# Optimization experiments

Hardware: AMD Instinct MI355X
Metric: run time of the kernel (lower is better)

## Reference

```python
import jax, jax.numpy as jnp
import numpy as np

B, V, N, S, F, H, K, STEPS = 8, 3, 400, 1200, 16, 32, 10, 12
ALPHA_FUSE = 0.8
NEG = -9e15


def setup_inputs() -> dict:
    key = jax.random.key(0)
    ks = jax.random.split(key, 16)
    g = lambda i, shape, s=0.1: jax.random.normal(ks[i], shape, jnp.float32) * s
    return {
        "feat": jax.random.normal(ks[0], (B, S, F), jnp.float32),
        "adj": jax.random.bernoulli(ks[1], 0.05, (B, V, S, S)).astype(jnp.float32),
        "dis_lab": jax.random.uniform(ks[2], (B, K), dtype=jnp.float32),
        "W_gat": g(3, (V, F, H), 0.3),
        "a_gat": g(4, (V, 2 * H, 1), 0.3),
        "qkv_W": g(5, (H, 3 * H)),
        "qkv_b": jnp.zeros((3 * H,), jnp.float32),
        "o_W": g(6, (H, H)),
        "o_b": jnp.zeros((H,), jnp.float32),
        "fus_W": g(7, (H, H)),
        "fus_b": jnp.zeros((H,), jnp.float32),
        "att1_W": g(8, (2 * H, H)),
        "att1_b": jnp.zeros((H,), jnp.float32),
        "att2_W": g(9, (H, 1)),
        "att2_b": jnp.zeros((1,), jnp.float32),
        "gru_Wih": g(10, (H, 3 * H)),
        "gru_Whh": g(11, (H, 3 * H)),
        "gru_bih": jnp.zeros((3 * H,), jnp.float32),
        "gru_bhh": jnp.zeros((3 * H,), jnp.float32),
        "out_W": g(12, (H, 1)),
        "out_b": jnp.zeros((1,), jnp.float32),
    }


def _forward(feat, adj, dis_lab, W_gat, a_gat, qkv_W, qkv_b, o_W, o_b,
             fus_W, fus_b, att1_W, att1_b, att2_W, att2_b,
             gru_Wih, gru_Whh, gru_bih, gru_bhh, out_W, out_b):
    # ---- per-view GAT (masked softmax over dense adjacency) ----
    Wh = jnp.einsum('bsf,vfh->bvsh', feat, W_gat)            # [B,V,S,H]
    a1, a2 = a_gat[:, :H, 0], a_gat[:, H:, 0]
    e = (jnp.einsum('bvsh,vh->bvs', Wh, a1)[..., :, None]
         + jnp.einsum('bvsh,vh->bvs', Wh, a2)[..., None, :])  # [B,V,S,S]
    e = jax.nn.leaky_relu(e, 0.2)
    e = jnp.where(adj > 0, e, NEG)
    att = jax.nn.softmax(e, axis=-1)
    hid = jax.nn.elu(jnp.einsum('bvst,bvth->bvsh', att, Wh))  # [B,V,S,H]
    # ---- cross-view self-attention fusion (single head) ----
    x = hid.reshape(B, V * S, H)
    q, k, v = jnp.split(x @ qkv_W + qkv_b, 3, axis=-1)
    logits = jnp.einsum('bld,bmd->blm', q, k) / jnp.sqrt(jnp.float32(H))
    sa = jnp.einsum('blm,bmd->bld', jax.nn.softmax(logits, axis=-1), v)
    sa = sa @ o_W + o_b
    hfuse = (ALPHA_FUSE * sa + (1.0 - ALPHA_FUSE) * x).reshape(B, V, S, H)
    gate = jax.nn.sigmoid(hfuse @ fus_W + fus_b)
    fusion = jnp.sum(gate * hfuse, axis=1)[:, 2 * N:, :]      # [B,N,H]
    # ---- attention over label stations ----
    label = fusion[:, :K, :]                                  # [B,K,H]
    unlabel = fusion[:, K, :]                                 # [B,H]
    cat = jnp.concatenate([label, jnp.broadcast_to(unlabel[:, None, :], label.shape)], axis=-1)
    s = jax.nn.relu(cat @ att1_W + att1_b) @ att2_W + att2_b  # [B,K,1]
    score = jax.nn.softmax(s[..., 0] * dis_lab, axis=1)
    ctx = jnp.einsum('bk,bkh->bh', score, label)
    # ---- GRU decoder (feed hidden state back as next input) ----
    def gru_cell(xt, h):
        gi = xt @ gru_Wih + gru_bih
        gh = h @ gru_Whh + gru_bhh
        ir, iz, inn = jnp.split(gi, 3, axis=-1)
        hr, hz, hn = jnp.split(gh, 3, axis=-1)
        r = jax.nn.sigmoid(ir + hr)
        z = jax.nn.sigmoid(iz + hz)
        n = jnp.tanh(inn + r * hn)
        return (1.0 - z) * n + z * h
    def step(carry, _):
        xt, h = carry
        h2 = gru_cell(xt, h)
        out = h2 @ out_W + out_b
        return (h2, h2), out[:, 0]
    _, outs = jax.lax.scan(step, (ctx, unlabel), None, length=STEPS)
    return outs.T  # [B, STEPS]


def reference(feat, adj, dis_lab, W_gat, a_gat, qkv_W, qkv_b, o_W, o_b,
              fus_W, fus_b, att1_W, att1_b, att2_W, att2_b,
              gru_Wih, gru_Whh, gru_bih, gru_bhh, out_W, out_b):
    return _forward(feat, adj, dis_lab, W_gat, a_gat, qkv_W, qkv_b, o_W, o_b,
                    fus_W, fus_b, att1_W, att1_b, att2_W, att2_b,
                    gru_Wih, gru_Whh, gru_bih, gru_bhh, out_W, out_b)
```

## Files before the change

kernel.cpp:

```cpp
#include <hip/hip_runtime.h>
#include <math.h>

#define Bb 8
#define Vv 3
#define Ss 1200
#define Ff 16
#define Hh 32
#define Kk 10
#define STEPS 12
#define ROWS (Bb*Vv*Ss)
#define L (Vv*Ss)
#define KPAD 1216

typedef __attribute__((ext_vector_type(8))) short bf16x8;
typedef __attribute__((ext_vector_type(4))) float f32x4;
typedef __attribute__((ext_vector_type(4))) unsigned int u32x4;

__device__ __forceinline__ unsigned int pack_hi2(float x0, float x1) {
    return (__float_as_uint(x1) & 0xFFFF0000u) | (__float_as_uint(x0) >> 16);
}
__device__ __forceinline__ unsigned int pack_lo2(float x0, float x1) {
    float h0 = __uint_as_float(__float_as_uint(x0) & 0xFFFF0000u);
    float h1 = __uint_as_float(__float_as_uint(x1) & 0xFFFF0000u);
    return (__float_as_uint(x1 - h1) & 0xFFFF0000u) | (__float_as_uint(x0 - h0) >> 16);
}

__global__ __launch_bounds__(256) void gat_wh_k(const float* __restrict__ feat,
                                                const float* __restrict__ W_gat,
                                                const float* __restrict__ a_gat,
                                                float* __restrict__ Wh,
                                                float* __restrict__ fvec,
                                                float* __restrict__ gvec) {
    int blk = blockIdx.x;
    int c = blk % 150;
    int v = (blk / 150) % Vv;
    int b = blk / (150 * Vv);
    int tid = threadIdx.x;
    int r = tid >> 5;
    int h = tid & 31;
    int s = c * 8 + r;

    __shared__ float Wg[16][32];
    __shared__ float fe[8][16];
    for (int i = tid; i < 512; i += 256) Wg[i >> 5][i & 31] = W_gat[v * 512 + i];
    for (int i = tid; i < 128; i += 256) fe[i >> 4][i & 15] = feat[(b * Ss + c * 8) * Ff + i];
    __syncthreads();

    float acc = 0.f;
#pragma unroll
    for (int k = 0; k < 16; ++k) acc += fe[r][k] * Wg[k][h];

    int row = (b * Vv + v) * Ss + s;
    Wh[(size_t)row * Hh + h] = acc;

    float a1 = a_gat[v * 64 + h];
    float a2 = a_gat[v * 64 + 32 + h];
    float pf = acc * a1, pg = acc * a2;
#pragma unroll
    for (int m = 16; m >= 1; m >>= 1) {
        pf += __shfl_xor(pf, m);
        pg += __shfl_xor(pg, m);
    }
    if (h == 0) { fvec[row] = pf; gvec[row] = pg; }
}

__global__ __launch_bounds__(256) void gmax_k(const float* __restrict__ gvec,
                                              float* __restrict__ Gmax) {
    int bv = blockIdx.x;
    int tid = threadIdx.x;
    float m = -3.0e38f;
    for (int t = tid; t < Ss; t += 256) m = fmaxf(m, gvec[bv * Ss + t]);
#pragma unroll
    for (int mm = 32; mm >= 1; mm >>= 1) m = fmaxf(m, __shfl_xor(m, mm));
    __shared__ float red[4];
    if ((tid & 63) == 0) red[tid >> 6] = m;
    __syncthreads();
    if (tid == 0) Gmax[bv] = fmaxf(fmaxf(red[0], red[1]), fmaxf(red[2], red[3]));
}

__global__ __launch_bounds__(256) void wht_k(const float* __restrict__ Wh,
                                             ushort* __restrict__ WhT_hi,
                                             ushort* __restrict__ WhT_lo) {
    int bv = blockIdx.x / 19, t = blockIdx.x % 19;
    int s0 = t * 64;
    int tid = threadIdx.x;
    __shared__ float T[64][33];
    for (int idx = tid; idx < 2048; idx += 256) {
        int r = idx >> 5, h = idx & 31;
        T[r][h] = (s0 + r < Ss) ? Wh[((size_t)bv * Ss + s0 + r) * Hh + h] : 0.f;
    }
    __syncthreads();
    int h = tid >> 3, c = tid & 7;
    unsigned int hb[4], lb[4];
#pragma unroll
    for (int j = 0; j < 4; ++j) {
        float e0 = T[c * 8 + 2 * j][h], e1 = T[c * 8 + 2 * j + 1][h];
        hb[j] = pack_hi2(e0, e1);
        lb[j] = pack_lo2(e0, e1);
    }
    size_t off = ((size_t)bv * 32 + h) * KPAD + s0 + c * 8;
    *(uint4*)(WhT_hi + off) = make_uint4(hb[0], hb[1], hb[2], hb[3]);
    *(uint4*)(WhT_lo + off) = make_uint4(lb[0], lb[1], lb[2], lb[3]);
}

__global__ __launch_bounds__(128) void wsplit_k(const float* __restrict__ qkv_W,
                                                ushort* __restrict__ WqT_hi,
                                                ushort* __restrict__ WqT_lo) {
    int n = threadIdx.x;
    if (n < 96) {
        for (int k = 0; k < 32; ++k) {
            float w = qkv_W[k * 96 + n];
            unsigned int u = __float_as_uint(w);
            float hf = __uint_as_float(u & 0xFFFF0000u);
            WqT_hi[n * 32 + k] = (ushort)(u >> 16);
            WqT_lo[n * 32 + k] = (ushort)(__float_as_uint(w - hf) >> 16);
        }
    }
}

__global__ __launch_bounds__(128) void gat_mfma_k(const float* __restrict__ adj,
                                                  const ushort* __restrict__ WhT_hi,
                                                  const ushort* __restrict__ WhT_lo,
                                                  const float* __restrict__ fvec,
                                                  const float* __restrict__ gvec,
                                                  const float* __restrict__ Gmax,
                                                  const ushort* __restrict__ WqT_hi,
                                                  const ushort* __restrict__ WqT_lo,
                                                  const float* __restrict__ qkv_b,
                                                  float* __restrict__ KV,
                                                  float* __restrict__ qsel,
                                                  float* __restrict__ hsel) {
    int blk = blockIdx.x;
    int bv = blk / 38, tb = blk % 38;
    int wave = threadIdx.x >> 6, lane = threadIdx.x & 63;
    int rowbase = tb * 32 + wave * 16;
    int lr = lane & 15, kg = lane >> 4;
    int b = bv / Vv, v = bv - b * Vv;

    int ar = rowbase + lr;
    int ar_c = (ar < Ss) ? ar : (Ss - 1);
    const float* adj_r = adj + ((size_t)bv * Ss + ar_c) * Ss;
    const float* g_b = gvec + (size_t)bv * Ss;
    float fr = fvec[bv * Ss + ar_c];
    float M = fr + Gmax[bv];
    float Mr = fmaxf(M, 0.2f * M);

    f32x4 acc0 = {0.f, 0.f, 0.f, 0.f}, acc1 = {0.f, 0.f, 0.f, 0.f};
    float psum = 0.f;
    const ushort* Bh0 = WhT_hi + ((size_t)bv * 32 + lr) * KPAD;
    const ushort* Bl0 = WhT_lo + ((size_t)bv * 32 + lr) * KPAD;

    for (int k0 = 0; k0 < KPAD; k0 += 32) {
        int t0 = k0 + kg * 8;
        bf16x8 bh0 = *(const bf16x8*)(Bh0 + t0);
        bf16x8 bl0 = *(const bf16x8*)(Bl0 + t0);
        bf16x8 bh1 = *(const bf16x8*)(Bh0 + 16 * KPAD + t0);
        bf16x8 bl1 = *(const bf16x8*)(Bl0 + 16 * KPAD + t0);

        float p[8];
        if (t0 < Ss) {
            float4 aA = *(const float4*)(adj_r + t0);
            float4 aB = *(const float4*)(adj_r + t0 + 4);
            float4 gA = *(const float4*)(g_b + t0);
            float4 gB = *(const float4*)(g_b + t0 + 4);
            float av[8] = {aA.x, aA.y, aA.z, aA.w, aB.x, aB.y, aB.z, aB.w};
            float gv[8] = {gA.x, gA.y, gA.z, gA.w, gB.x, gB.y, gB.z, gB.w};
#pragma unroll
            for (int j = 0; j < 8; ++j) {
                float e = fr + gv[j];
                e = fmaxf(e, 0.2f * e);
                float pe = __expf(e - Mr);
                p[j] = (av[j] > 0.f) ? pe : 0.f;
                psum += p[j];
            }
        } else {
#pragma unroll
            for (int j = 0; j < 8; ++j) p[j] = 0.f;
        }
        unsigned int hb[4], lb[4];
#pragma unroll
        for (int j = 0; j < 4; ++j) {
            hb[j] = pack_hi2(p[2 * j], p[2 * j + 1]);
            lb[j] = pack_lo2(p[2 * j], p[2 * j + 1]);
        }
        bf16x8 ah = __builtin_bit_cast(bf16x8, (u32x4){hb[0], hb[1], hb[2], hb[3]});
        bf16x8 al = __builtin_bit_cast(bf16x8, (u32x4){lb[0], lb[1], lb[2], lb[3]});
        acc0 = __builtin_amdgcn_mfma_f32_16x16x32_bf16(ah, bh0, acc0, 0, 0, 0);
        acc0 = __builtin_amdgcn_mfma_f32_16x16x32_bf16(ah, bl0, acc0, 0, 0, 0);
        acc0 = __builtin_amdgcn_mfma_f32_16x16x32_bf16(al, bh0, acc0, 0, 0, 0);
        acc1 = __builtin_amdgcn_mfma_f32_16x16x32_bf16(ah, bh1, acc1, 0, 0, 0);
        acc1 = __builtin_amdgcn_mfma_f32_16x16x32_bf16(ah, bl1, acc1, 0, 0, 0);
        acc1 = __builtin_amdgcn_mfma_f32_16x16x32_bf16(al, bh1, acc1, 0, 0, 0);
    }

    psum += __shfl_xor(psum, 16);
    psum += __shfl_xor(psum, 32);

    __shared__ float hidS[2][16][36];
#pragma unroll
    for (int j = 0; j < 4; ++j) {
        float ps = __shfl(psum, kg * 4 + j);
        float r0 = acc0[j] / ps;
        float r1 = acc1[j] / ps;
        hidS[wave][kg * 4 + j][lr]      = (r0 > 0.f) ? r0 : expm1f(r0);
        hidS[wave][kg * 4 + j][16 + lr] = (r1 > 0.f) ? r1 : expm1f(r1);
    }
    __syncthreads();

    float4 h4a = *(const float4*)&hidS[wave][lr][8 * kg];
    float4 h4b = *(const float4*)&hidS[wave][lr][8 * kg + 4];
    float hv[8] = {h4a.x, h4a.y, h4a.z, h4a.w, h4b.x, h4b.y, h4b.z, h4b.w};
    unsigned int hhb[4], hlb[4];
#pragma unroll
    for (int j = 0; j < 4; ++j) {
        hhb[j] = pack_hi2(hv[2 * j], hv[2 * j + 1]);
        hlb[j] = pack_lo2(hv[2 * j], hv[2 * j + 1]);
    }
    bf16x8 ahh = __builtin_bit_cast(bf16x8, (u32x4){hhb[0], hhb[1], hhb[2], hhb[3]});
    bf16x8 ahl = __builtin_bit_cast(bf16x8, (u32x4){hlb[0], hlb[1], hlb[2], hlb[3]});

#pragma unroll
    for (int t = 0; t < 4; ++t) {
        int n = 32 + t * 16 + lr;
        bf16x8 wh = *(const bf16x8*)(WqT_hi + n * 32 + 8 * kg);
        bf16x8 wl = *(const bf16x8*)(WqT_lo + n * 32 + 8 * kg);
        float bias = qkv_b[n];
        f32x4 qa = {bias, bias, bias, bias};
        qa = __builtin_amdgcn_mfma_f32_16x16x32_bf16(ahh, wh, qa, 0, 0, 0);
        qa = __builtin_amdgcn_mfma_f32_16x16x32_bf16(ahh, wl, qa, 0, 0, 0);
        qa = __builtin_amdgcn_mfma_f32_16x16x32_bf16(ahl, wh, qa, 0, 0, 0);
#pragma unroll
        for (int j = 0; j < 4; ++j) {
            int row = rowbase + kg * 4 + j;
            if (row < Ss)
                KV[((size_t)b * L + v * Ss + row) * 64 + t * 16 + lr] = qa[j];
        }
    }
    if (rowbase == 800) {
#pragma unroll
        for (int t = 0; t < 2; ++t) {
            int n = t * 16 + lr;
            bf16x8 wh = *(const bf16x8*)(WqT_hi + n * 32 + 8 * kg);
            bf16x8 wl = *(const bf16x8*)(WqT_lo + n * 32 + 8 * kg);
            float bias = qkv_b[n];
            f32x4 qa = {bias, bias, bias, bias};
            qa = __builtin_amdgcn_mfma_f32_16x16x32_bf16(ahh, wh, qa, 0, 0, 0);
            qa = __builtin_amdgcn_mfma_f32_16x16x32_bf16(ahh, wl, qa, 0, 0, 0);
            qa = __builtin_amdgcn_mfma_f32_16x16x32_bf16(ahl, wh, qa, 0, 0, 0);
#pragma unroll
            for (int j = 0; j < 4; ++j) {
                int si = kg * 4 + j;
                if (si < 11)
                    qsel[((size_t)b * 33 + si * 3 + v) * 32 + t * 16 + lr] = qa[j];
            }
        }
#pragma unroll
        for (int j = 0; j < 4; ++j) {
            int si = kg * 4 + j;
            if (si < 11) {
                hsel[(((size_t)b * Vv + v) * 11 + si) * 32 + lr]      = hidS[wave][si][lr];
                hsel[(((size_t)b * Vv + v) * 11 + si) * 32 + 16 + lr] = hidS[wave][si][16 + lr];
            }
        }
    }
}

#define CH 120
#define NCH 30
#define PREC 34
__global__ __launch_bounds__(256) void attn_part_k(const float* __restrict__ KV,
                                                   const float* __restrict__ qsel,
                                                   float* __restrict__ part) {
    int blk = blockIdx.x;
    int b = blk / NCH, ch = blk % NCH;
    int k0 = ch * CH;
    int tid = threadIdx.x;
    const float inv = 0.1767766952966369f;

    __shared__ float qS[33][33];
    __shared__ float kS[CH][33];
    __shared__ float lS[33][124];
    __shared__ float mS[33], lsS[33];

    for (int idx = tid; idx < 33 * 32; idx += 256) {
        int q = idx >> 5, i = idx & 31;
        qS[q][i] = qsel[((size_t)b * 33 + q) * 32 + i];
    }
    for (int idx = tid; idx < CH * 32; idx += 256) {
        int r = idx >> 5, i = idx & 31;
        kS[r][i] = KV[((size_t)b * L + k0 + r) * 64 + i];
    }
    __syncthreads();

    for (int idx = tid; idx < 33 * CH; idx += 256) {
        int q = idx / CH, k = idx - q * CH;
        float d = 0.f;
#pragma unroll
        for (int i = 0; i < 32; ++i) d += qS[q][i] * kS[k][i];
        lS[q][k] = d * inv;
    }
    __syncthreads();

    int q4 = tid >> 2, j4 = tid & 3;
    if (q4 < 33) {
        float m = -3.0e38f;
        for (int k = j4; k < CH; k += 4) m = fmaxf(m, lS[q4][k]);
        m = fmaxf(m, __shfl_xor(m, 1));
        m = fmaxf(m, __shfl_xor(m, 2));
        float ssum = 0.f;
        for (int k = j4; k < CH; k += 4) {
            float p = __expf(lS[q4][k] - m);
            lS[q4][k] = p;
            ssum += p;
        }
        ssum += __shfl_xor(ssum, 1);
        ssum += __shfl_xor(ssum, 2);
        if (j4 == 0) { mS[q4] = m; lsS[q4] = ssum; }
    }
    __syncthreads();

    for (int idx = tid; idx < CH * 32; idx += 256) {
        int r = idx >> 5, i = idx & 31;
        kS[r][i] = KV[((size_t)b * L + k0 + r) * 64 + 32 + i];
    }
    __syncthreads();

    float* po = part + ((size_t)b * NCH + ch) * (33 * PREC);
    for (int idx = tid; idx < 33 * 32; idx += 256) {
        int q = idx >> 5, hh = idx & 31;
        float a = 0.f;
        for (int k = 0; k < CH; k += 4) {
            float4 p4 = *(const float4*)&lS[q][k];
            a += p4.x * kS[k][hh] + p4.y * kS[k+1][hh] + p4.z * kS[k+2][hh] + p4.w * kS[k+3][hh];
        }
        po[q * PREC + hh] = a;
    }
    if (tid < 33) { po[tid * PREC + 32] = mS[tid]; po[tid * PREC + 33] = lsS[tid]; }
}

__global__ __launch_bounds__(256) void attn_comb_k(const float* __restrict__ part,
                                                   const float* __restrict__ hsel,
                                                   const float* __restrict__ o_W,
                                                   const float* __restrict__ o_b,
                                                   const float* __restrict__ fus_W,
                                                   const float* __restrict__ fus_b,
                                                   float* __restrict__ hfg) {
    int b = blockIdx.x;
    int tid = threadIdx.x;
    __shared__ float RS[33][NCH];
    __shared__ float LSs[33];
    __shared__ float oS[33][33];
    __shared__ float hfS[33][33];
    const float* pb = part + (size_t)b * NCH * (33 * PREC);

    if (tid < 33) {
        float M = -3.0e38f;
        for (int c = 0; c < NCH; ++c) M = fmaxf(M, pb[c * 33 * PREC + tid * PREC + 32]);
        float Lt = 0.f;
        for (int c = 0; c < NCH; ++c) {
            float w = __expf(pb[c * 33 * PREC + tid * PREC + 32] - M);
            RS[tid][c] = w;
            Lt += w * pb[c * 33 * PREC + tid * PREC + 33];
        }
        LSs[tid] = Lt;
    }
    __syncthreads();

    for (int idx = tid; idx < 33 * 32; idx += 256) {
        int q = idx >> 5, hh = idx & 31;
        float a = 0.f;
        for (int c = 0; c < NCH; ++c) a += RS[q][c] * pb[c * 33 * PREC + q * PREC + hh];
        oS[q][hh] = a / LSs[q];
    }
    __syncthreads();
    for (int idx = tid; idx < 33 * 32; idx += 256) {
        int q = idx >> 5, hh = idx & 31;
        int si = q / 3, v = q - si * 3;
        float o = o_b[hh];
#pragma unroll
        for (int i = 0; i < 32; ++i) o += oS[q][i] * o_W[i * 32 + hh];
        float x = hsel[(((size_t)b * Vv + v) * 11 + si) * Hh + hh];
        hfS[q][hh] = 0.8f * o + 0.2f * x;
    }
    __syncthreads();
    for (int idx = tid; idx < 33 * 32; idx += 256) {
        int q = idx >> 5, hh = idx & 31;
        float gacc = fus_b[hh];
#pragma unroll
        for (int i = 0; i < 32; ++i) gacc += hfS[q][i] * fus_W[i * 32 + hh];
        float gate = 1.f / (1.f + __expf(-gacc));
        hfg[(size_t)(b * 33 + q) * 32 + hh] = gate * hfS[q][hh];
    }
}

__global__ __launch_bounds__(64) void head_k(const float* __restrict__ hfg,
                                             const float* __restrict__ dis_lab,
                                             const float* __restrict__ att1_W,
                                             const float* __restrict__ att1_b,
                                             const float* __restrict__ att2_W,
                                             const float* __restrict__ att2_b,
                                             const float* __restrict__ Wih,
                                             const float* __restrict__ Whh,
                                             const float* __restrict__ bih,
                                             const float* __restrict__ bhh,
                                             const float* __restrict__ out_W,
                                             const float* __restrict__ out_b,
                                             float* __restrict__ out) {
    int b = blockIdx.x;
    int tid = threadIdx.x;
    int j = tid & 31, half = tid >> 5;

    __shared__ float lab[11][32];
    __shared__ float a1T[32][68];
    __shared__ float WihT[3][32][36];
    __shared__ float WhhT[3][32][36];
    __shared__ float sc[12];
    __shared__ float xS[32], hS[32];

    for (int i = tid; i < 352; i += 64) {
        int k = i >> 5, hh = i & 31;
        float val = 0.f;
#pragma unroll
        for (int v = 0; v < 3; ++v) val += hfg[(size_t)(b * 33 + k * 3 + v) * 32 + hh];
        lab[k][hh] = val;
    }
    for (int idx = tid; idx < 2048; idx += 64) {
        int i = idx >> 5, jj = idx & 31;
        a1T[jj][i] = att1_W[idx];
    }
    for (int idx = tid; idx < 3072; idx += 64) {
        int i = idx / 96, col = idx - i * 96;
        int g = col >> 5, jj = col & 31;
        WihT[g][jj][i] = Wih[idx];
        WhhT[g][jj][i] = Whh[idx];
    }
    __syncthreads();

    float a2w = att2_W[j];
    float a1b = att1_b[j];
    float a2b = att2_b[0];
#pragma unroll
    for (int kk = 0; kk < 5; ++kk) {
        int k = 2 * kk + half;
        float t1 = a1b;
#pragma unroll
        for (int c = 0; c < 8; ++c) {
            float4 lb4 = *(const float4*)&lab[k][c * 4];
            float4 w4  = *(const float4*)&a1T[j][c * 4];
            t1 += lb4.x * w4.x + lb4.y * w4.y + lb4.z * w4.z + lb4.w * w4.w;
        }
#pragma unroll
        for (int c = 0; c < 8; ++c) {
            float4 lb4 = *(const float4*)&lab[10][c * 4];
            float4 w4  = *(const float4*)&a1T[j][32 + c * 4];
            t1 += lb4.x * w4.x + lb4.y * w4.y + lb4.z * w4.z + lb4.w * w4.w;
        }
        float val = fmaxf(t1, 0.f) * a2w;
#pragma unroll
        for (int mm = 16; mm >= 1; mm >>= 1) val += __shfl_xor(val, mm);
        if (j == 0) sc[k] = (val + a2b) * dis_lab[b * Kk + k];
    }
    __syncthreads();
    if (tid == 0) {
        float mx = sc[0];
        for (int k = 1; k < 10; ++k) mx = fmaxf(mx, sc[k]);
        float sm = 0.f;
        for (int k = 0; k < 10; ++k) { sc[k] = __expf(sc[k] - mx); sm += sc[k]; }
        for (int k = 0; k < 10; ++k) sc[k] /= sm;
    }
    __syncthreads();
    if (tid < 32) {
        float c = 0.f;
        for (int k = 0; k < 10; ++k) c += sc[k] * lab[k][tid];
        xS[tid] = c;
        hS[tid] = lab[10][tid];
    }
    __syncthreads();

    float b_ir = bih[j], b_iz = bih[32 + j], b_in = bih[64 + j];
    float b_hr = bhh[j], b_hz = bhh[32 + j], b_hn = bhh[64 + j];
    float ow = out_W[j], ob = out_b[0];
    int i0 = half * 16;

    for (int t = 0; t < STEPS; ++t) {
        float gi_r = 0.f, gi_z = 0.f, gi_n = 0.f;
        float gh_r = 0.f, gh_z = 0.f, gh_n = 0.f;
#pragma unroll
        for (int c = 0; c < 4; ++c) {
            float4 x4 = *(const float4*)&xS[i0 + c * 4];
            float4 h4 = *(const float4*)&hS[i0 + c * 4];
            float4 wr = *(const float4*)&WihT[0][j][i0 + c * 4];
            float4 wz = *(const float4*)&WihT[1][j][i0 + c * 4];
            float4 wn = *(const float4*)&WihT[2][j][i0 + c * 4];
            float4 ur = *(const float4*)&WhhT[0][j][i0 + c * 4];
            float4 uz = *(const float4*)&WhhT[1][j][i0 + c * 4];
            float4 un = *(const float4*)&WhhT[2][j][i0 + c * 4];
            gi_r += x4.x * wr.x + x4.y * wr.y + x4.z * wr.z + x4.w * wr.w;
            gi_z += x4.x * wz.x + x4.y * wz.y + x4.z * wz.z + x4.w * wz.w;
            gi_n += x4.x * wn.x + x4.y * wn.y + x4.z * wn.z + x4.w * wn.w;
            gh_r += h4.x * ur.x + h4.y * ur.y + h4.z * ur.z + h4.w * ur.w;
            gh_z += h4.x * uz.x + h4.y * uz.y + h4.z * uz.z + h4.w * uz.w;
            gh_n += h4.x * un.x + h4.y * un.y + h4.z * un.z + h4.w * un.w;
        }
        gi_r += __shfl_xor(gi_r, 32); gi_z += __shfl_xor(gi_z, 32); gi_n += __shfl_xor(gi_n, 32);
        gh_r += __shfl_xor(gh_r, 32); gh_z += __shfl_xor(gh_z, 32); gh_n += __shfl_xor(gh_n, 32);

        float hprev = hS[j];
        float r = 1.f / (1.f + __expf(-(gi_r + b_ir + gh_r + b_hr)));
        float z = 1.f / (1.f + __expf(-(gi_z + b_iz + gh_z + b_hz)));
        float n = tanhf(gi_n + b_in + r * (gh_n + b_hn));
        float hnew = (1.f - z) * n + z * hprev;

        float outp = hnew * ow;
#pragma unroll
        for (int mm = 16; mm >= 1; mm >>= 1) outp += __shfl_xor(outp, mm);
        if (tid == 0) out[b * STEPS + t] = outp + ob;
        __syncthreads();
        if (tid < 32) { hS[tid] = hnew; xS[tid] = hnew; }
        __syncthreads();
    }
}

extern "C" void kernel_launch(void* const* d_in, const int* in_sizes, int n_in,
                              void* d_out, int out_size, void* d_ws, size_t ws_size,
                              hipStream_t stream) {
    const float* feat    = (const float*)d_in[0];
    const float* adj     = (const float*)d_in[1];
    const float* dis_lab = (const float*)d_in[2];
    const float* W_gat   = (const float*)d_in[3];
    const float* a_gat   = (const float*)d_in[4];
    const float* qkv_W   = (const float*)d_in[5];
    const float* qkv_b   = (const float*)d_in[6];
    const float* o_W     = (const float*)d_in[7];
    const float* o_b     = (const float*)d_in[8];
    const float* fus_W   = (const float*)d_in[9];
    const float* fus_b   = (const float*)d_in[10];
    const float* att1_W  = (const float*)d_in[11];
    const float* att1_b  = (const float*)d_in[12];
    const float* att2_W  = (const float*)d_in[13];
    const float* att2_b  = (const float*)d_in[14];
    const float* Wih     = (const float*)d_in[15];
    const float* Whh     = (const float*)d_in[16];
    const float* bih     = (const float*)d_in[17];
    const float* bhh     = (const float*)d_in[18];
    const float* out_W   = (const float*)d_in[19];
    const float* out_b   = (const float*)d_in[20];
    float* out = (float*)d_out;

    float* ws = (float*)d_ws;
    float*  Wh     = ws;
    float*  KV     = ws;
    float*  fvec   = ws + 1843200;
    float*  gvec   = ws + 1872000;
    float*  Gmax   = ws + 1900800;
    ushort* WhT_hi = (ushort*)(ws + 1900832);
    float*  part   = ws + 1900832;
    ushort* WhT_lo = (ushort*)(ws + 2367776);
    float*  qsel   = ws + 2834720;
    float*  hsel   = ws + 2843168;
    float*  hfg    = ws + 2851616;
    ushort* WqT_hi = (ushort*)(ws + 2860064);
    ushort* WqT_lo = (ushort*)(ws + 2861600);

    gat_wh_k<<<dim3(Bb * Vv * 150), dim3(256), 0, stream>>>(feat, W_gat, a_gat, Wh, fvec, gvec);
    gmax_k<<<dim3(Bb * Vv), dim3(256), 0, stream>>>(gvec, Gmax);
    wht_k<<<dim3(Bb * Vv * 19), dim3(256), 0, stream>>>(Wh, WhT_hi, WhT_lo);
    wsplit_k<<<dim3(1), dim3(128), 0, stream>>>(qkv_W, WqT_hi, WqT_lo);
    gat_mfma_k<<<dim3(Bb * Vv * 38), dim3(128), 0, stream>>>(adj, WhT_hi, WhT_lo,
                                                             fvec, gvec, Gmax,
                                                             WqT_hi, WqT_lo, qkv_b,
                                                             KV, qsel, hsel);
    attn_part_k<<<dim3(Bb * NCH), dim3(256), 0, stream>>>(KV, qsel, part);
    attn_comb_k<<<dim3(Bb), dim3(256), 0, stream>>>(part, hsel, o_W, o_b, fus_W, fus_b, hfg);
    head_k<<<dim3(Bb), dim3(64), 0, stream>>>(hfg, dis_lab, att1_W, att1_b, att2_W, att2_b,
                                              Wih, Whh, bih, bhh, out_W, out_b, out);
}
```

Baseline: 137.5 us.

## Fold QKV projections into attention and split GAT K-loop across waves

Attention no longer materializes K and V for every row. Queries are projected through Wk once (qt and qc), logits are taken directly against the GAT hidden states, and the V projection is applied after the softmax-weighted sum by linearity. The adjacency is packed into a bitmask by a new kernel. The GAT aggregation kernel now uses 16-row tiles with four waves splitting the K range, reducing partial accumulators through shared memory. This drops the large KV buffer and the wsplit kernel, but adds an extra kernel launch and still reads the full adjacency once.

```diff
diff --git a/kernel.cpp b/kernel.cpp
--- a/kernel.cpp
+++ b/kernel.cpp
@@ -11,6 +11,7 @@
 #define ROWS (Bb*Vv*Ss)
 #define L (Vv*Ss)
 #define KPAD 1216
+#define MW 38
 
 typedef __attribute__((ext_vector_type(8))) short bf16x8;
 typedef __attribute__((ext_vector_type(4))) float f32x4;
@@ -103,45 +104,46 @@
     *(uint4*)(WhT_lo + off) = make_uint4(lb[0], lb[1], lb[2], lb[3]);
 }
 
-__global__ __launch_bounds__(128) void wsplit_k(const float* __restrict__ qkv_W,
-                                                ushort* __restrict__ WqT_hi,
-                                                ushort* __restrict__ WqT_lo) {
-    int n = threadIdx.x;
-    if (n < 96) {
-        for (int k = 0; k < 32; ++k) {
-            float w = qkv_W[k * 96 + n];
-            unsigned int u = __float_as_uint(w);
-            float hf = __uint_as_float(u & 0xFFFF0000u);
-            WqT_hi[n * 32 + k] = (ushort)(u >> 16);
-            WqT_lo[n * 32 + k] = (ushort)(__float_as_uint(w - hf) >> 16);
-        }
-    }
-}
-
-__global__ __launch_bounds__(128) void gat_mfma_k(const float* __restrict__ adj,
+__global__ __launch_bounds__(320) void adj_pack_k(const float* __restrict__ adj,
+                                                  unsigned int* __restrict__ maskb) {
+    int row = blockIdx.x;
+    int tid = threadIdx.x;
+    __shared__ unsigned char nib[320];
+    unsigned char n = 0;
+    if (tid < 300) {
+        float4 a = ((const float4*)(adj + (size_t)row * Ss))[tid];
+        n = (a.x > 0.f ? 1u : 0u) | (a.y > 0.f ? 2u : 0u) |
+            (a.z > 0.f ? 4u : 0u) | (a.w > 0.f ? 8u : 0u);
+    }
+    nib[tid] = n;
+    __syncthreads();
+    if (tid < MW) {
+        unsigned int m = 0;
+#pragma unroll
+        for (int i = 0; i < 8; ++i) m |= ((unsigned int)nib[tid * 8 + i]) << (4 * i);
+        maskb[(size_t)row * MW + tid] = m;
+    }
+}
+
+__global__ __launch_bounds__(256) void gat_mfma_k(const unsigned int* __restrict__ maskb,
                                                   const ushort* __restrict__ WhT_hi,
                                                   const ushort* __restrict__ WhT_lo,
                                                   const float* __restrict__ fvec,
                                                   const float* __restrict__ gvec,
                                                   const float* __restrict__ Gmax,
-                                                  const ushort* __restrict__ WqT_hi,
-                                                  const ushort* __restrict__ WqT_lo,
-                                                  const float* __restrict__ qkv_b,
-                                                  float* __restrict__ KV,
-                                                  float* __restrict__ qsel,
+                                                  float* __restrict__ hid,
                                                   float* __restrict__ hsel) {
     int blk = blockIdx.x;
-    int bv = blk / 38, tb = blk % 38;
-    int wave = threadIdx.x >> 6, lane = threadIdx.x & 63;
-    int rowbase = tb * 32 + wave * 16;
+    int bv = blk / 75, tb = blk % 75;
+    int wk = threadIdx.x >> 6, lane = threadIdx.x & 63;
+    int rowbase = tb * 16;
     int lr = lane & 15, kg = lane >> 4;
     int b = bv / Vv, v = bv - b * Vv;
 
     int ar = rowbase + lr;
-    int ar_c = (ar < Ss) ? ar : (Ss - 1);
-    const float* adj_r = adj + ((size_t)bv * Ss + ar_c) * Ss;
     const float* g_b = gvec + (size_t)bv * Ss;
-    float fr = fvec[bv * Ss + ar_c];
+    const unsigned int* mrow = maskb + (size_t)(bv * Ss + ar) * MW;
+    float fr = fvec[bv * Ss + ar];
     float M = fr + Gmax[bv];
     float Mr = fmaxf(M, 0.2f * M);
 
@@ -150,32 +152,34 @@
     const ushort* Bh0 = WhT_hi + ((size_t)bv * 32 + lr) * KPAD;
     const ushort* Bl0 = WhT_lo + ((size_t)bv * 32 + lr) * KPAD;
 
-    for (int k0 = 0; k0 < KPAD; k0 += 32) {
+    int kst = wk * 320;
+    int kend = kst + 320; if (kend > KPAD) kend = KPAD;
+    for (int k0 = kst; k0 < kend; k0 += 32) {
         int t0 = k0 + kg * 8;
         bf16x8 bh0 = *(const bf16x8*)(Bh0 + t0);
         bf16x8 bl0 = *(const bf16x8*)(Bl0 + t0);
         bf16x8 bh1 = *(const bf16x8*)(Bh0 + 16 * KPAD + t0);
         bf16x8 bl1 = *(const bf16x8*)(Bl0 + 16 * KPAD + t0);
 
-        float p[8];
-        if (t0 < Ss) {
-            float4 aA = *(const float4*)(adj_r + t0);
-            float4 aB = *(const float4*)(adj_r + t0 + 4);
+        unsigned int mbyte = (mrow[k0 >> 5] >> (kg * 8)) & 0xFFu;
+        float gv8[8];
+        if (t0 + 8 <= Ss) {
             float4 gA = *(const float4*)(g_b + t0);
             float4 gB = *(const float4*)(g_b + t0 + 4);
-            float av[8] = {aA.x, aA.y, aA.z, aA.w, aB.x, aB.y, aB.z, aB.w};
-            float gv[8] = {gA.x, gA.y, gA.z, gA.w, gB.x, gB.y, gB.z, gB.w};
-#pragma unroll
-            for (int j = 0; j < 8; ++j) {
-                float e = fr + gv[j];
-                e = fmaxf(e, 0.2f * e);
-                float pe = __expf(e - Mr);
-                p[j] = (av[j] > 0.f) ? pe : 0.f;
-                psum += p[j];
-            }
+            gv8[0] = gA.x; gv8[1] = gA.y; gv8[2] = gA.z; gv8[3] = gA.w;
+            gv8[4] = gB.x; gv8[5] = gB.y; gv8[6] = gB.z; gv8[7] = gB.w;
         } else {
 #pragma unroll
-            for (int j = 0; j < 8; ++j) p[j] = 0.f;
+            for (int j = 0; j < 8; ++j) gv8[j] = (t0 + j < Ss) ? g_b[t0 + j] : 0.f;
+        }
+        float p[8];
+#pragma unroll
+        for (int j = 0; j < 8; ++j) {
+            float e = fr + gv8[j];
+            e = fmaxf(e, 0.2f * e);
+            float pe = __expf(e - Mr);
+            p[j] = ((mbyte >> j) & 1u) ? pe : 0.f;
+            psum += p[j];
         }
         unsigned int hb[4], lb[4];
 #pragma unroll
@@ -196,80 +200,37 @@
     psum += __shfl_xor(psum, 16);
     psum += __shfl_xor(psum, 32);
 
-    __shared__ float hidS[2][16][36];
+    __shared__ float accS[4][2][16][17];
+    __shared__ float psS[4][16];
 #pragma unroll
     for (int j = 0; j < 4; ++j) {
-        float ps = __shfl(psum, kg * 4 + j);
-        float r0 = acc0[j] / ps;
-        float r1 = acc1[j] / ps;
-        hidS[wave][kg * 4 + j][lr]      = (r0 > 0.f) ? r0 : expm1f(r0);
-        hidS[wave][kg * 4 + j][16 + lr] = (r1 > 0.f) ? r1 : expm1f(r1);
-    }
-    __syncthreads();
-
-    float4 h4a = *(const float4*)&hidS[wave][lr][8 * kg];
-    float4 h4b = *(const float4*)&hidS[wave][lr][8 * kg + 4];
-    float hv[8] = {h4a.x, h4a.y, h4a.z, h4a.w, h4b.x, h4b.y, h4b.z, h4b.w};
-    unsigned int hhb[4], hlb[4];
-#pragma unroll
-    for (int j = 0; j < 4; ++j) {
-        hhb[j] = pack_hi2(hv[2 * j], hv[2 * j + 1]);
-        hlb[j] = pack_lo2(hv[2 * j], hv[2 * j + 1]);
-    }
-    bf16x8 ahh = __builtin_bit_cast(bf16x8, (u32x4){hhb[0], hhb[1], hhb[2], hhb[3]});
-    bf16x8 ahl = __builtin_bit_cast(bf16x8, (u32x4){hlb[0], hlb[1], hlb[2], hlb[3]});
-
-#pragma unroll
-    for (int t = 0; t < 4; ++t) {
-        int n = 32 + t * 16 + lr;
-        bf16x8 wh = *(const bf16x8*)(WqT_hi + n * 32 + 8 * kg);
-        bf16x8 wl = *(const bf16x8*)(WqT_lo + n * 32 + 8 * kg);
-        float bias = qkv_b[n];
-        f32x4 qa = {bias, bias, bias, bias};
-        qa = __builtin_amdgcn_mfma_f32_16x16x32_bf16(ahh, wh, qa, 0, 0, 0);
-        qa = __builtin_amdgcn_mfma_f32_16x16x32_bf16(ahh, wl, qa, 0, 0, 0);
-        qa = __builtin_amdgcn_mfma_f32_16x16x32_bf16(ahl, wh, qa, 0, 0, 0);
-#pragma unroll
-        for (int j = 0; j < 4; ++j) {
-            int row = rowbase + kg * 4 + j;
-            if (row < Ss)
-                KV[((size_t)b * L + v * Ss + row) * 64 + t * 16 + lr] = qa[j];
-        }
-    }
-    if (rowbase == 800) {
-#pragma unroll
-        for (int t = 0; t < 2; ++t) {
-            int n = t * 16 + lr;
-            bf16x8 wh = *(const bf16x8*)(WqT_hi + n * 32 + 8 * kg);
-            bf16x8 wl = *(const bf16x8*)(WqT_lo + n * 32 + 8 * kg);
-            float bias = qkv_b[n];
-            f32x4 qa = {bias, bias, bias, bias};
-            qa = __builtin_amdgcn_mfma_f32_16x16x32_bf16(ahh, wh, qa, 0, 0, 0);
-            qa = __builtin_amdgcn_mfma_f32_16x16x32_bf16(ahh, wl, qa, 0, 0, 0);
-            qa = __builtin_amdgcn_mfma_f32_16x16x32_bf16(ahl, wh, qa, 0, 0, 0);
-#pragma unroll
-            for (int j = 0; j < 4; ++j) {
-                int si = kg * 4 + j;
-                if (si < 11)
-                    qsel[((size_t)b * 33 + si * 3 + v) * 32 + t * 16 + lr] = qa[j];
-            }
-        }
-#pragma unroll
-        for (int j = 0; j < 4; ++j) {
-            int si = kg * 4 + j;
-            if (si < 11) {
-                hsel[(((size_t)b * Vv + v) * 11 + si) * 32 + lr]      = hidS[wave][si][lr];
-                hsel[(((size_t)b * Vv + v) * 11 + si) * 32 + 16 + lr] = hidS[wave][si][16 + lr];
-            }
-        }
+        accS[wk][0][kg * 4 + j][lr] = acc0[j];
+        accS[wk][1][kg * 4 + j][lr] = acc1[j];
+    }
+    if (lane < 16) psS[wk][lr] = psum;
+    __syncthreads();
+    if (threadIdx.x < 16)
+        psS[0][threadIdx.x] += psS[1][threadIdx.x] + psS[2][threadIdx.x] + psS[3][threadIdx.x];
+    __syncthreads();
+
+    bool qb = (tb == 50);
+    for (int idx = threadIdx.x; idx < 512; idx += 256) {
+        int r = idx >> 5, col = idx & 31, tt = col >> 4, c = col & 15;
+        float a = accS[0][tt][r][c] + accS[1][tt][r][c] + accS[2][tt][r][c] + accS[3][tt][r][c];
+        float rr = a / psS[0][r];
+        float hv = (rr > 0.f) ? rr : expm1f(rr);
+        hid[((size_t)bv * Ss + rowbase + r) * 32 + col] = hv;
+        if (qb && r < 11) hsel[(((size_t)b * Vv + v) * 11 + r) * 32 + col] = hv;
     }
 }
 
 #define CH 120
 #define NCH 30
 #define PREC 34
-__global__ __launch_bounds__(256) void attn_part_k(const float* __restrict__ KV,
-                                                   const float* __restrict__ qsel,
+__global__ __launch_bounds__(256) void attn_part_k(const float* __restrict__ hid,
+                                                   const float* __restrict__ hsel,
+                                                   const float* __restrict__ qkv_W,
+                                                   const float* __restrict__ qkv_b,
                                                    float* __restrict__ part) {
     int blk = blockIdx.x;
     int b = blk / NCH, ch = blk % NCH;
@@ -277,27 +238,59 @@
     int tid = threadIdx.x;
     const float inv = 0.1767766952966369f;
 
+    __shared__ float hC[CH][33];
+    __shared__ float hq[33][33];
+    __shared__ float W1[32][33];
+    __shared__ float W2[32][33];
     __shared__ float qS[33][33];
-    __shared__ float kS[CH][33];
+    __shared__ float qt[33][33];
+    __shared__ float qc[33];
     __shared__ float lS[33][124];
     __shared__ float mS[33], lsS[33];
 
-    for (int idx = tid; idx < 33 * 32; idx += 256) {
-        int q = idx >> 5, i = idx & 31;
-        qS[q][i] = qsel[((size_t)b * 33 + q) * 32 + i];
-    }
     for (int idx = tid; idx < CH * 32; idx += 256) {
         int r = idx >> 5, i = idx & 31;
-        kS[r][i] = KV[((size_t)b * L + k0 + r) * 64 + i];
+        hC[r][i] = hid[((size_t)b * L + k0 + r) * 32 + i];
+    }
+    for (int idx = tid; idx < 33 * 32; idx += 256) {
+        int q = idx >> 5, i = idx & 31;
+        int si = q / 3, v = q - si * 3;
+        hq[q][i] = hsel[(((size_t)b * Vv + v) * 11 + si) * 32 + i];
+    }
+    for (int idx = tid; idx < 1024; idx += 256) {
+        int i = idx >> 5, j = idx & 31;
+        W1[i][j] = qkv_W[i * 96 + j];
+        W2[i][j] = qkv_W[i * 96 + 32 + j];
+    }
+    __syncthreads();
+    for (int idx = tid; idx < 33 * 32; idx += 256) {
+        int q = idx >> 5, j = idx & 31;
+        float a = qkv_b[j];
+#pragma unroll
+        for (int i = 0; i < 32; ++i) a += hq[q][i] * W1[i][j];
+        qS[q][j] = a;
+    }
+    __syncthreads();
+    for (int idx = tid; idx < 33 * 32; idx += 256) {
+        int q = idx >> 5, i = idx & 31;
+        float a = 0.f;
+#pragma unroll
+        for (int j = 0; j < 32; ++j) a += qS[q][j] * W2[i][j];
+        qt[q][i] = a;
+    }
+    if (tid < 33) {
+        float a = 0.f;
+        for (int j = 0; j < 32; ++j) a += qS[tid][j] * qkv_b[32 + j];
+        qc[tid] = a;
     }
     __syncthreads();
 
     for (int idx = tid; idx < 33 * CH; idx += 256) {
-        int q = idx / CH, k = idx - q * CH;
+        int q = idx / CH, m = idx - q * CH;
         float d = 0.f;
 #pragma unroll
-        for (int i = 0; i < 32; ++i) d += qS[q][i] * kS[k][i];
-        lS[q][k] = d * inv;
+        for (int i = 0; i < 32; ++i) d += qt[q][i] * hC[m][i];
+        lS[q][m] = (d + qc[q]) * inv;
     }
     __syncthreads();
 
@@ -319,19 +312,13 @@
     }
     __syncthreads();
 
-    for (int idx = tid; idx < CH * 32; idx += 256) {
-        int r = idx >> 5, i = idx & 31;
-        kS[r][i] = KV[((size_t)b * L + k0 + r) * 64 + 32 + i];
-    }
-    __syncthreads();
-
     float* po = part + ((size_t)b * NCH + ch) * (33 * PREC);
     for (int idx = tid; idx < 33 * 32; idx += 256) {
         int q = idx >> 5, hh = idx & 31;
         float a = 0.f;
         for (int k = 0; k < CH; k += 4) {
             float4 p4 = *(const float4*)&lS[q][k];
-            a += p4.x * kS[k][hh] + p4.y * kS[k+1][hh] + p4.z * kS[k+2][hh] + p4.w * kS[k+3][hh];
+            a += p4.x * hC[k][hh] + p4.y * hC[k+1][hh] + p4.z * hC[k+2][hh] + p4.w * hC[k+3][hh];
         }
         po[q * PREC + hh] = a;
     }
@@ -340,6 +327,8 @@
 
 __global__ __launch_bounds__(256) void attn_comb_k(const float* __restrict__ part,
                                                    const float* __restrict__ hsel,
+                                                   const float* __restrict__ qkv_W,
+                                                   const float* __restrict__ qkv_b,
                                                    const float* __restrict__ o_W,
                                                    const float* __restrict__ o_b,
                                                    const float* __restrict__ fus_W,
@@ -350,6 +339,7 @@
     __shared__ float RS[33][NCH];
     __shared__ float LSs[33];
     __shared__ float oS[33][33];
+    __shared__ float vS[33][33];
     __shared__ float hfS[33][33];
     const float* pb = part + (size_t)b * NCH * (33 * PREC);
 
@@ -374,11 +364,19 @@
     }
     __syncthreads();
     for (int idx = tid; idx < 33 * 32; idx += 256) {
+        int q = idx >> 5, j = idx & 31;
+        float a = qkv_b[64 + j];
+#pragma unroll
+        for (int i = 0; i < 32; ++i) a += oS[q][i] * qkv_W[i * 96 + 64 + j];
+        vS[q][j] = a;
+    }
+    __syncthreads();
+    for (int idx = tid; idx < 33 * 32; idx += 256) {
         int q = idx >> 5, hh = idx & 31;
         int si = q / 3, v = q - si * 3;
         float o = o_b[hh];
 #pragma unroll
-        for (int i = 0; i < 32; ++i) o += oS[q][i] * o_W[i * 32 + hh];
+        for (int i = 0; i < 32; ++i) o += vS[q][i] * o_W[i * 32 + hh];
         float x = hsel[(((size_t)b * Vv + v) * 11 + si) * Hh + hh];
         hfS[q][hh] = 0.8f * o + 0.2f * x;
     }
@@ -549,29 +547,26 @@
 
     float* ws = (float*)d_ws;
     float*  Wh     = ws;
-    float*  KV     = ws;
-    float*  fvec   = ws + 1843200;
-    float*  gvec   = ws + 1872000;
-    float*  Gmax   = ws + 1900800;
-    ushort* WhT_hi = (ushort*)(ws + 1900832);
-    float*  part   = ws + 1900832;
-    ushort* WhT_lo = (ushort*)(ws + 2367776);
-    float*  qsel   = ws + 2834720;
-    float*  hsel   = ws + 2843168;
-    float*  hfg    = ws + 2851616;
-    ushort* WqT_hi = (ushort*)(ws + 2860064);
-    ushort* WqT_lo = (ushort*)(ws + 2861600);
+    float*  hid    = ws;
+    float*  fvec   = ws + 921600;
+    float*  gvec   = ws + 950400;
+    float*  Gmax   = ws + 979200;
+    ushort* WhT_hi = (ushort*)(ws + 979232);
+    float*  part   = ws + 979232;
+    ushort* WhT_lo = (ushort*)(ws + 1446176);
+    float*  hsel   = ws + 1913120;
+    float*  hfg    = ws + 1921568;
+    unsigned int* maskb = (unsigned int*)(ws + 1930016);
 
     gat_wh_k<<<dim3(Bb * Vv * 150), dim3(256), 0, stream>>>(feat, W_gat, a_gat, Wh, fvec, gvec);
     gmax_k<<<dim3(Bb * Vv), dim3(256), 0, stream>>>(gvec, Gmax);
     wht_k<<<dim3(Bb * Vv * 19), dim3(256), 0, stream>>>(Wh, WhT_hi, WhT_lo);
-    wsplit_k<<<dim3(1), dim3(128), 0, stream>>>(qkv_W, WqT_hi, WqT_lo);
-    gat_mfma_k<<<dim3(Bb * Vv * 38), dim3(128), 0, stream>>>(adj, WhT_hi, WhT_lo,
-                                                             fvec, gvec, Gmax,
-                                                             WqT_hi, WqT_lo, qkv_b,
-                                                             KV, qsel, hsel);
-    attn_part_k<<<dim3(Bb * NCH), dim3(256), 0, stream>>>(KV, qsel, part);
-    attn_comb_k<<<dim3(Bb), dim3(256), 0, stream>>>(part, hsel, o_W, o_b, fus_W, fus_b, hfg);
+    adj_pack_k<<<dim3(ROWS), dim3(320), 0, stream>>>(adj, maskb);
+    gat_mfma_k<<<dim3(Bb * Vv * 75), dim3(256), 0, stream>>>(maskb, WhT_hi, WhT_lo,
+                                                             fvec, gvec, Gmax, hid, hsel);
+    attn_part_k<<<dim3(Bb * NCH), dim3(256), 0, stream>>>(hid, hsel, qkv_W, qkv_b, part);
+    attn_comb_k<<<dim3(Bb), dim3(256), 0, stream>>>(part, hsel, qkv_W, qkv_b,
+                                                    o_W, o_b, fus_W, fus_b, hfg);
     head_k<<<dim3(Bb), dim3(64), 0, stream>>>(hfg, dis_lab, att1_W, att1_b, att2_W, att2_b,
                                               Wih, Whh, bih, bhh, out_W, out_b, out);
 }
```

Result: slower. 149.9 us (+9.0%).
